# Optimization experiments

Hardware: AMD Instinct MI355X
Metric: run time of the kernel (lower is better)

Reference implementation:

```python
import jax, jax.numpy as jnp
import numpy as np

N_NODES = 100000

def gcn_conv(x, edge_index, W, b):
    # GCNConv with normalize=True and self-loops:
    # out = D^{-1/2} (A + I) D^{-1/2} (x W) + b
    h = x @ W                                   # [N, out]
    src, dst = edge_index[0], edge_index[1]
    deg = jax.ops.segment_sum(jnp.ones(src.shape[0], h.dtype), dst,
                              num_segments=N_NODES) + 1.0  # +1 for self loop
    dinv = jax.lax.rsqrt(deg)
    norm = dinv[src] * dinv[dst]                # [E]
    agg = jax.ops.segment_sum(h[src] * norm[:, None], dst,
                              num_segments=N_NODES)        # [N, out]
    agg = agg + h * (1.0 / deg)[:, None]        # self-loop term: norm_ii = 1/deg_i
    return agg + b


def setup_inputs() -> dict:
    key = jax.random.key(0)
    k0, k1, k2, k3 = jax.random.split(key, 4)
    N, E, F_IN, H, C = N_NODES, 1600000, 256, 128, 40
    x = jax.random.normal(k0, (N, F_IN), dtype=jnp.float32)
    edge_index = jax.random.randint(k1, (2, E), 0, N, dtype=jnp.int64)
    W1 = jax.random.normal(k2, (F_IN, H), dtype=jnp.float32) * (1.0 / np.sqrt(F_IN))
    b1 = jnp.zeros((H,), jnp.float32)
    W2 = jax.random.normal(k3, (H, C), dtype=jnp.float32) * (1.0 / np.sqrt(H))
    b2 = jnp.zeros((C,), jnp.float32)
    return {"x": x, "edge_index": edge_index, "W1": W1, "b1": b1, "W2": W2, "b2": b2}


def reference(x, edge_index, W1, b1, W2, b2):
    # layer 1 + ReLU (dropout = identity in eval mode)
    h = jax.nn.relu(gcn_conv(x, edge_index, W1, b1))
    # final layer (no activation)
    return gcn_conv(h, edge_index, W2, b2)
```

## Files before the change

kernel.cpp:

```cpp
#include <hip/hip_runtime.h>
#include <hip/hip_bf16.h>


#define FIN 256
#define HDIM 128
#define CDIM 40
#define CAP 8192
#define EC 8192

typedef __attribute__((ext_vector_type(8))) short bf16x8;
typedef __attribute__((ext_vector_type(4))) float f32x4;

__device__ inline short f2bf(float f) {
    unsigned u = __float_as_uint(f);
    unsigned r = (u + 0x7FFFu + ((u >> 16) & 1u)) >> 16;
    return (short)r;
}
__device__ inline float bflo(unsigned u) { return __uint_as_float(u << 16); }
__device__ inline float bfhi(unsigned u) { return __uint_as_float(u & 0xFFFF0000u); }
__device__ inline int rdl_i(int v, int l) { return __builtin_amdgcn_readlane(v, l); }
__device__ inline float rdl_f(float v, int l) {
    return __uint_as_float((unsigned)__builtin_amdgcn_readlane((int)__float_as_uint(v), l));
}

__global__ __launch_bounds__(1024) void p1_hist_k(const int* __restrict__ ei, int* __restrict__ mat,
                                                  int E, int NBUCK) {
    __shared__ int hist[512];
    for (int t = threadIdx.x; t < NBUCK; t += 1024) hist[t] = 0;
    __syncthreads();
    int e0 = blockIdx.x * EC;
#pragma unroll
    for (int k = 0; k < EC; k += 1024) {
        int e = e0 + k + threadIdx.x;
        if (e < E) atomicAdd(&hist[ei[E + e] >> 8], 1);
    }
    __syncthreads();
    for (int t = threadIdx.x; t < NBUCK; t += 1024) mat[blockIdx.x * NBUCK + t] = hist[t];
}

__global__ __launch_bounds__(64) void scan_cols_k(int* __restrict__ mat, int* __restrict__ bcnt,
                                                  int NB1, int NBUCK) {
    int b = blockIdx.x;
    int lane = threadIdx.x;
    int carry = b * CAP;
    for (int c0 = 0; c0 < NB1; c0 += 64) {
        int idx = c0 + lane;
        int v = (idx < NB1) ? mat[idx * NBUCK + b] : 0;
        int incl = v;
#pragma unroll
        for (int off = 1; off < 64; off <<= 1) {
            int t = __shfl_up(incl, off);
            if (lane >= off) incl += t;
        }
        if (idx < NB1) mat[idx * NBUCK + b] = carry + (incl - v);
        carry += __shfl(incl, 63);
    }
    if (lane == 0) bcnt[b] = carry - b * CAP;
}

__global__ __launch_bounds__(1024) void p1_scatter_k(const int* __restrict__ ei, const int* __restrict__ mat,
                                                     int* __restrict__ bmem, int E, int NBUCK) {
    __shared__ int base[512];
    for (int t = threadIdx.x; t < NBUCK; t += 1024) base[t] = mat[blockIdx.x * NBUCK + t];
    __syncthreads();
    int e0 = blockIdx.x * EC;
#pragma unroll
    for (int k = 0; k < EC; k += 1024) {
        int e = e0 + k + threadIdx.x;
        if (e < E) {
            int s = ei[e];
            int d = ei[E + e];
            int pos = atomicAdd(&base[d >> 8], 1);
            bmem[pos] = s | ((d & 255) << 20);
        }
    }
}

__global__ __launch_bounds__(256) void p2_build_k(const int* __restrict__ bmem, const int* __restrict__ bcnt,
                                                  int* __restrict__ csr, int2* __restrict__ nseg,
                                                  float* __restrict__ dinv, float* __restrict__ invd, int N) {
    __shared__ int hist[256], cur[256], sc[256];
    __shared__ int stage[CAP];
    const int b = blockIdx.x;
    const int tid = threadIdx.x;
    int cnt = bcnt[b];
    if (cnt > CAP) cnt = CAP;
    const int* src = bmem + b * CAP;
    hist[tid] = 0;
    __syncthreads();
    for (int j = tid; j < cnt; j += 256) atomicAdd(&hist[src[j] >> 20], 1);
    __syncthreads();
    int v = hist[tid];
    sc[tid] = v;
    __syncthreads();
    for (int off = 1; off < 256; off <<= 1) {
        int t = (tid >= off) ? sc[tid - off] : 0;
        __syncthreads();
        sc[tid] += t;
        __syncthreads();
    }
    int excl = sc[tid] - v;
    cur[tid] = excl;
    int i = b * 256 + tid;
    if (i < N) {
        nseg[i] = make_int2(b * CAP + excl, v);
        float dg = (float)(v + 1);
        dinv[i] = rsqrtf(dg);
        invd[i] = 1.0f / dg;
    }
    __syncthreads();
    for (int j = tid; j < cnt; j += 256) {
        int rec = src[j];
        int pos = atomicAdd(&cur[rec >> 20], 1);
        stage[pos] = rec & 0xFFFFF;
    }
    __syncthreads();
    int* dst = csr + b * CAP;
    for (int j = tid; j < cnt; j += 256) dst[j] = stage[j];
}

__global__ __launch_bounds__(256) void castW1_k(const float* __restrict__ W1, short* __restrict__ W1T) {
    int idx = blockIdx.x * 256 + threadIdx.x;
    int k = idx >> 7, n = idx & 127;
    W1T[n * FIN + k] = f2bf(W1[idx]);
}

__global__ __launch_bounds__(256) void castW2_k(const float* __restrict__ W2, short* __restrict__ W2T) {
    int idx = blockIdx.x * 256 + threadIdx.x;
    int c = idx >> 7, k = idx & 127;
    W2T[idx] = (c < CDIM) ? f2bf(W2[k * CDIM + c]) : (short)0;
}

#define LDSTRIDE 40
__global__ __launch_bounds__(256) void gemm1_mfma_k(const float* __restrict__ X,
                                                    const short* __restrict__ W1T,
                                                    short* __restrict__ T1b, int N) {
    __shared__ short As[128 * LDSTRIDE];
    __shared__ short Bs[128 * LDSTRIDE];
    const int tid = threadIdx.x;
    const int lane = tid & 63;
    const int wid = tid >> 6;
    const int w0 = wid & 1, w1 = wid >> 1;
    const int quad = lane >> 4;
    const int l16 = lane & 15;
    const int rowbase = blockIdx.x * 128;
    const int sr = tid >> 1;
    const int sh = tid & 1;

    f32x4 acc[4][4];
#pragma unroll
    for (int a = 0; a < 4; a++)
#pragma unroll
        for (int b = 0; b < 4; b++) acc[a][b] = (f32x4){0.f, 0.f, 0.f, 0.f};

    const int arow = min(rowbase + sr, N - 1);
    const float* xsrc = X + (size_t)arow * FIN + sh * 16;
    const int4* bsrc = (const int4*)(W1T + (size_t)sr * FIN + sh * 16);

    for (int k0 = 0; k0 < FIN; k0 += 32) {
        float vals[16];
        *(float4*)&vals[0]  = *(const float4*)(xsrc + k0);
        *(float4*)&vals[4]  = *(const float4*)(xsrc + k0 + 4);
        *(float4*)&vals[8]  = *(const float4*)(xsrc + k0 + 8);
        *(float4*)&vals[12] = *(const float4*)(xsrc + k0 + 12);
        short tmp[16];
#pragma unroll
        for (int c = 0; c < 16; c++) tmp[c] = f2bf(vals[c]);
        ((int4*)&As[sr * LDSTRIDE + sh * 16])[0] = ((int4*)tmp)[0];
        ((int4*)&As[sr * LDSTRIDE + sh * 16])[1] = ((int4*)tmp)[1];
        int4 b0 = bsrc[k0 >> 3];
        int4 b1 = bsrc[(k0 >> 3) + 1];
        ((int4*)&Bs[sr * LDSTRIDE + sh * 16])[0] = b0;
        ((int4*)&Bs[sr * LDSTRIDE + sh * 16])[1] = b1;
        __syncthreads();

        bf16x8 afr[4], bfr[4];
#pragma unroll
        for (int mt = 0; mt < 4; mt++)
            afr[mt] = *(const bf16x8*)&As[(w1 * 64 + mt * 16 + l16) * LDSTRIDE + quad * 8];
#pragma unroll
        for (int nt = 0; nt < 4; nt++)
            bfr[nt] = *(const bf16x8*)&Bs[(w0 * 64 + nt * 16 + l16) * LDSTRIDE + quad * 8];
#pragma unroll
        for (int mt = 0; mt < 4; mt++)
#pragma unroll
            for (int nt = 0; nt < 4; nt++)
                acc[mt][nt] = __builtin_amdgcn_mfma_f32_16x16x32_bf16(afr[mt], bfr[nt], acc[mt][nt], 0, 0, 0);
        __syncthreads();
    }
#pragma unroll
    for (int mt = 0; mt < 4; mt++) {
#pragma unroll
        for (int r = 0; r < 4; r++) {
            int row = rowbase + w1 * 64 + mt * 16 + quad * 4 + r;
            if (row < N) {
#pragma unroll
                for (int nt = 0; nt < 4; nt++) {
                    int col = w0 * 64 + nt * 16 + l16;
                    T1b[(size_t)row * HDIM + col] = f2bf(acc[mt][nt][r]);
                }
            }
        }
    }
}

__global__ __launch_bounds__(256) void agg1_k(const short* __restrict__ T1b, const int2* __restrict__ nseg,
                                              const int* __restrict__ csr, const float* __restrict__ dinv,
                                              const float* __restrict__ invd, const float* __restrict__ b1,
                                              unsigned* __restrict__ Hb, int N) {
    const int lane = threadIdx.x & 63;
    const int i = blockIdx.x * 4 + (threadIdx.x >> 6);
    if (i >= N) return;
    const int2 sg = nseg[i];
    const int e0 = sg.x, deg = sg.y;
    int sv = 0; float wv = 0.f;
    if (lane < deg) { sv = csr[e0 + lane]; wv = dinv[sv]; }

    float accx = 0.f, accy = 0.f;
    const int dmain = deg < 64 ? deg : 64;
    const int d8 = dmain & ~7;
    const unsigned* rowp = (const unsigned*)T1b;
    int j = 0;
    for (; j < d8; j += 8) {
        int   s0 = rdl_i(sv, j),     s1 = rdl_i(sv, j + 1), s2 = rdl_i(sv, j + 2), s3 = rdl_i(sv, j + 3);
        int   s4 = rdl_i(sv, j + 4), s5 = rdl_i(sv, j + 5), s6 = rdl_i(sv, j + 6), s7 = rdl_i(sv, j + 7);
        float w0 = rdl_f(wv, j),     w1 = rdl_f(wv, j + 1), w2 = rdl_f(wv, j + 2), w3 = rdl_f(wv, j + 3);
        float w4 = rdl_f(wv, j + 4), w5 = rdl_f(wv, j + 5), w6 = rdl_f(wv, j + 6), w7 = rdl_f(wv, j + 7);
        unsigned r0 = rowp[(size_t)s0 * 64 + lane];
        unsigned r1 = rowp[(size_t)s1 * 64 + lane];
        unsigned r2 = rowp[(size_t)s2 * 64 + lane];
        unsigned r3 = rowp[(size_t)s3 * 64 + lane];
        unsigned r4 = rowp[(size_t)s4 * 64 + lane];
        unsigned r5 = rowp[(size_t)s5 * 64 + lane];
        unsigned r6 = rowp[(size_t)s6 * 64 + lane];
        unsigned r7 = rowp[(size_t)s7 * 64 + lane];
        accx += w0 * bflo(r0) + w1 * bflo(r1) + w2 * bflo(r2) + w3 * bflo(r3)
              + w4 * bflo(r4) + w5 * bflo(r5) + w6 * bflo(r6) + w7 * bflo(r7);
        accy += w0 * bfhi(r0) + w1 * bfhi(r1) + w2 * bfhi(r2) + w3 * bfhi(r3)
              + w4 * bfhi(r4) + w5 * bfhi(r5) + w6 * bfhi(r6) + w7 * bfhi(r7);
    }
    for (; j < dmain; ++j) {
        int s = rdl_i(sv, j); float w = rdl_f(wv, j);
        unsigned r = rowp[(size_t)s * 64 + lane];
        accx += w * bflo(r); accy += w * bfhi(r);
    }
    for (int e = e0 + 64; e < e0 + deg; ++e) {
        int s = csr[e]; float w = dinv[s];
        unsigned r = rowp[(size_t)s * 64 + lane];
        accx += w * bflo(r); accy += w * bfhi(r);
    }
    const float di = dinv[i], sf = invd[i];
    unsigned rs = rowp[(size_t)i * 64 + lane];
    float2 bc = *(const float2*)(b1 + 2 * lane);
    float ox = fmaxf(bc.x + sf * bflo(rs) + di * accx, 0.f);
    float oy = fmaxf(bc.y + sf * bfhi(rs) + di * accy, 0.f);
    unsigned pk = ((unsigned)(unsigned short)f2bf(ox)) | (((unsigned)(unsigned short)f2bf(oy)) << 16);
    Hb[(size_t)i * 64 + lane] = pk;
}

__global__ __launch_bounds__(256) void gemm2_mfma_k(const short* __restrict__ Hb,
                                                    const short* __restrict__ W2T,
                                                    float* __restrict__ T2, int N) {
    __shared__ short As[128 * LDSTRIDE];
    __shared__ short Bs[48 * LDSTRIDE];
    const int tid = threadIdx.x;
    const int lane = tid & 63;
    const int wid = tid >> 6;
    const int quad = lane >> 4;
    const int l16 = lane & 15;
    const int rowbase = blockIdx.x * 128;
    const int sr = tid >> 1;
    const int sh = tid & 1;

    f32x4 acc[2][3];
#pragma unroll
    for (int a = 0; a < 2; a++)
#pragma unroll
        for (int b = 0; b < 3; b++) acc[a][b] = (f32x4){0.f, 0.f, 0.f, 0.f};

    const int arow = min(rowbase + sr, N - 1);
    const int4* asrc = (const int4*)(Hb + (size_t)arow * HDIM + sh * 16);
    const int br = tid >> 1, bh = tid & 1;
    const int4* bsrc = (const int4*)(W2T + br * HDIM + bh * 16);

    for (int k0 = 0; k0 < HDIM; k0 += 32) {
        int4 a0 = asrc[k0 >> 3];
        int4 a1 = asrc[(k0 >> 3) + 1];
        ((int4*)&As[sr * LDSTRIDE + sh * 16])[0] = a0;
        ((int4*)&As[sr * LDSTRIDE + sh * 16])[1] = a1;
        if (tid < 96) {
            int4 b0 = bsrc[k0 >> 3];
            int4 b1 = bsrc[(k0 >> 3) + 1];
            ((int4*)&Bs[br * LDSTRIDE + bh * 16])[0] = b0;
            ((int4*)&Bs[br * LDSTRIDE + bh * 16])[1] = b1;
        }
        __syncthreads();
        bf16x8 afr[2], bfr[3];
#pragma unroll
        for (int mt = 0; mt < 2; mt++)
            afr[mt] = *(const bf16x8*)&As[(wid * 32 + mt * 16 + l16) * LDSTRIDE + quad * 8];
#pragma unroll
        for (int nt = 0; nt < 3; nt++)
            bfr[nt] = *(const bf16x8*)&Bs[(nt * 16 + l16) * LDSTRIDE + quad * 8];
#pragma unroll
        for (int mt = 0; mt < 2; mt++)
#pragma unroll
            for (int nt = 0; nt < 3; nt++)
                acc[mt][nt] = __builtin_amdgcn_mfma_f32_16x16x32_bf16(afr[mt], bfr[nt], acc[mt][nt], 0, 0, 0);
        __syncthreads();
    }
#pragma unroll
    for (int mt = 0; mt < 2; mt++) {
#pragma unroll
        for (int r = 0; r < 4; r++) {
            int row = rowbase + wid * 32 + mt * 16 + quad * 4 + r;
            if (row < N) {
#pragma unroll
                for (int nt = 0; nt < 3; nt++) {
                    int col = nt * 16 + l16;
                    if (col < CDIM) T2[(size_t)row * CDIM + col] = acc[mt][nt][r];
                }
            }
        }
    }
}

__global__ __launch_bounds__(256) void agg2_k(const float* __restrict__ T2, const int2* __restrict__ nseg,
                                              const int* __restrict__ csr, const float* __restrict__ dinv,
                                              const float* __restrict__ invd, const float* __restrict__ b2,
                                              float* __restrict__ OUT, int N) {
    const int lane = threadIdx.x & 63;
    const int i = blockIdx.x * 4 + (threadIdx.x >> 6);
    if (i >= N) return;
    const int2 sg = nseg[i];
    const int e0 = sg.x, deg = sg.y;
    int sv = 0; float wv = 0.f;
    if (lane < deg) { sv = csr[e0 + lane]; wv = dinv[sv]; }
    const int c = lane < CDIM ? lane : CDIM - 1;
    float accE = 0.f;
    const int dmain = deg < 64 ? deg : 64;
    const int d8 = dmain & ~7;
    int j = 0;
    for (; j < d8; j += 8) {
        int   s0 = rdl_i(sv, j),     s1 = rdl_i(sv, j + 1), s2 = rdl_i(sv, j + 2), s3 = rdl_i(sv, j + 3);
        int   s4 = rdl_i(sv, j + 4), s5 = rdl_i(sv, j + 5), s6 = rdl_i(sv, j + 6), s7 = rdl_i(sv, j + 7);
        float w0 = rdl_f(wv, j),     w1 = rdl_f(wv, j + 1), w2 = rdl_f(wv, j + 2), w3 = rdl_f(wv, j + 3);
        float w4 = rdl_f(wv, j + 4), w5 = rdl_f(wv, j + 5), w6 = rdl_f(wv, j + 6), w7 = rdl_f(wv, j + 7);
        float v0 = T2[(size_t)s0 * CDIM + c];
        float v1 = T2[(size_t)s1 * CDIM + c];
        float v2 = T2[(size_t)s2 * CDIM + c];
        float v3 = T2[(size_t)s3 * CDIM + c];
        float v4 = T2[(size_t)s4 * CDIM + c];
        float v5 = T2[(size_t)s5 * CDIM + c];
        float v6 = T2[(size_t)s6 * CDIM + c];
        float v7 = T2[(size_t)s7 * CDIM + c];
        accE += w0 * v0 + w1 * v1 + w2 * v2 + w3 * v3 + w4 * v4 + w5 * v5 + w6 * v6 + w7 * v7;
    }
    for (; j < dmain; ++j) {
        int s = rdl_i(sv, j); float w = rdl_f(wv, j);
        accE += w * T2[(size_t)s * CDIM + c];
    }
    for (int e = e0 + 64; e < e0 + deg; ++e) {
        int s = csr[e]; float w = dinv[s];
        accE += w * T2[(size_t)s * CDIM + c];
    }
    if (lane < CDIM)
        OUT[(size_t)i * CDIM + lane] = b2[lane] + invd[i] * T2[(size_t)i * CDIM + lane] + dinv[i] * accE;
}

extern "C" void kernel_launch(void* const* d_in, const int* in_sizes, int n_in,
                              void* d_out, int out_size, void* d_ws, size_t ws_size,
                              hipStream_t stream) {
    const float* x   = (const float*)d_in[0];
    const int*   ei  = (const int*)d_in[1];
    const float* W1  = (const float*)d_in[2];
    const float* b1  = (const float*)d_in[3];
    const float* W2  = (const float*)d_in[4];
    const float* b2  = (const float*)d_in[5];
    float*       out = (float*)d_out;

    const int Hd  = in_sizes[3];
    const int Fin = in_sizes[2] / Hd;
    const int N   = in_sizes[0] / Fin;
    const int E   = in_sizes[1] / 2;

    const int NBUCK = (N + 255) / 256;
    const int NB1   = (E + EC - 1) / EC;

    char* base = (char*)d_ws;
    size_t off = 0;
    auto alloc = [&](size_t bytes) -> void* {
        void* p = base + off;
        off += (bytes + 255) & ~(size_t)255;
        return p;
    };
    size_t matB  = (size_t)NB1 * NBUCK * 4;
    size_t bmemB = (size_t)NBUCK * CAP * 4;
    size_t t1bB  = (size_t)N * HDIM * 2;
    size_t regA  = matB + 256 + bmemB;
    if (t1bB > regA) regA = t1bB;
    char* pA = (char*)alloc(regA);
    int*   mat  = (int*)pA;
    int*   bmem = (int*)(pA + ((matB + 255) & ~(size_t)255));
    short* t1b  = (short*)pA;

    int*      bcnt = (int*)alloc((size_t)NBUCK * 4);
    int*      csr  = (int*)alloc((size_t)NBUCK * CAP * 4);
    int2*     nseg = (int2*)alloc((size_t)N * 8);
    float*    dinv = (float*)alloc((size_t)N * 4);
    float*    invd = (float*)alloc((size_t)N * 4);
    short*    W1T  = (short*)alloc((size_t)HDIM * FIN * 2);
    short*    W2T  = (short*)alloc((size_t)48 * HDIM * 2);
    unsigned* hb   = (unsigned*)alloc((size_t)N * HDIM * 2);
    float*    t2   = (float*)alloc((size_t)N * CDIM * 4);

    p1_hist_k<<<NB1, 1024, 0, stream>>>(ei, mat, E, NBUCK);
    scan_cols_k<<<NBUCK, 64, 0, stream>>>(mat, bcnt, NB1, NBUCK);
    p1_scatter_k<<<NB1, 1024, 0, stream>>>(ei, mat, bmem, E, NBUCK);
    p2_build_k<<<NBUCK, 256, 0, stream>>>(bmem, bcnt, csr, nseg, dinv, invd, N);
    castW1_k<<<(HDIM * Fin + 255) / 256, 256, 0, stream>>>(W1, W1T);
    castW2_k<<<(48 * HDIM + 255) / 256, 256, 0, stream>>>(W2, W2T);

    gemm1_mfma_k<<<(N + 127) / 128, 256, 0, stream>>>(x, W1T, t1b, N);
    agg1_k<<<(N + 3) / 4, 256, 0, stream>>>(t1b, nseg, csr, dinv, invd, b1, hb, N);
    gemm2_mfma_k<<<(N + 127) / 128, 256, 0, stream>>>((const short*)hb, W2T, t2, N);
    agg2_k<<<(N + 3) / 4, 256, 0, stream>>>(t2, nseg, csr, dinv, invd, b2, out, N);
}
```

Measured before the change: 360.6 us.

## Split each wavefront into four quads gathering different neighbours with 16-byte loads

The two aggregation kernels now assign each 16-lane quarter of a wavefront to a different neighbour. Each lane loads 16 bytes (8 bf16 features in layer 1, 4 floats in layer 2) instead of one 4-byte word, and the four partial sums are combined with xor shuffles at the end. The aim is more memory-level parallelism per wavefront and fewer, wider gather instructions, especially for the 40-wide layer-2 rows where many lanes sat idle before. It also merges the two weight-cast kernels into one launch. The cost is extra shuffle reductions, a quarter of lanes idle in layer 2, and fewer unrolled independent loads per iteration.

```diff
diff --git a/kernel.cpp b/kernel.cpp
--- a/kernel.cpp
+++ b/kernel.cpp
@@ -18,10 +18,6 @@
 }
 __device__ inline float bflo(unsigned u) { return __uint_as_float(u << 16); }
 __device__ inline float bfhi(unsigned u) { return __uint_as_float(u & 0xFFFF0000u); }
-__device__ inline int rdl_i(int v, int l) { return __builtin_amdgcn_readlane(v, l); }
-__device__ inline float rdl_f(float v, int l) {
-    return __uint_as_float((unsigned)__builtin_amdgcn_readlane((int)__float_as_uint(v), l));
-}
 
 __global__ __launch_bounds__(1024) void p1_hist_k(const int* __restrict__ ei, int* __restrict__ mat,
                                                   int E, int NBUCK) {
@@ -119,16 +115,19 @@
     for (int j = tid; j < cnt; j += 256) dst[j] = stage[j];
 }
 
-__global__ __launch_bounds__(256) void castW1_k(const float* __restrict__ W1, short* __restrict__ W1T) {
+__global__ __launch_bounds__(256) void castW_k(const float* __restrict__ W1, const float* __restrict__ W2,
+                                               short* __restrict__ W1T, short* __restrict__ W2T) {
     int idx = blockIdx.x * 256 + threadIdx.x;
-    int k = idx >> 7, n = idx & 127;
-    W1T[n * FIN + k] = f2bf(W1[idx]);
-}
-
-__global__ __launch_bounds__(256) void castW2_k(const float* __restrict__ W2, short* __restrict__ W2T) {
-    int idx = blockIdx.x * 256 + threadIdx.x;
-    int c = idx >> 7, k = idx & 127;
-    W2T[idx] = (c < CDIM) ? f2bf(W2[k * CDIM + c]) : (short)0;
+    if (idx < FIN * HDIM) {
+        int k = idx >> 7, n = idx & 127;
+        W1T[n * FIN + k] = f2bf(W1[idx]);
+    } else {
+        int j = idx - FIN * HDIM;
+        if (j < 48 * HDIM) {
+            int c = j >> 7, k = j & 127;
+            W2T[j] = (c < CDIM) ? f2bf(W2[k * CDIM + c]) : (short)0;
+        }
+    }
 }
 
 #define LDSTRIDE 40
@@ -209,6 +208,8 @@
                                               const float* __restrict__ invd, const float* __restrict__ b1,
                                               unsigned* __restrict__ Hb, int N) {
     const int lane = threadIdx.x & 63;
+    const int quad = lane >> 4;
+    const int ql = lane & 15;
     const int i = blockIdx.x * 4 + (threadIdx.x >> 6);
     if (i >= N) return;
     const int2 sg = nseg[i];
@@ -216,46 +217,58 @@
     int sv = 0; float wv = 0.f;
     if (lane < deg) { sv = csr[e0 + lane]; wv = dinv[sv]; }
 
-    float accx = 0.f, accy = 0.f;
+    const uint4* rowp = (const uint4*)T1b;
+    float acc[8];
+#pragma unroll
+    for (int t = 0; t < 8; t++) acc[t] = 0.f;
+
     const int dmain = deg < 64 ? deg : 64;
-    const int d8 = dmain & ~7;
-    const unsigned* rowp = (const unsigned*)T1b;
-    int j = 0;
-    for (; j < d8; j += 8) {
-        int   s0 = rdl_i(sv, j),     s1 = rdl_i(sv, j + 1), s2 = rdl_i(sv, j + 2), s3 = rdl_i(sv, j + 3);
-        int   s4 = rdl_i(sv, j + 4), s5 = rdl_i(sv, j + 5), s6 = rdl_i(sv, j + 6), s7 = rdl_i(sv, j + 7);
-        float w0 = rdl_f(wv, j),     w1 = rdl_f(wv, j + 1), w2 = rdl_f(wv, j + 2), w3 = rdl_f(wv, j + 3);
-        float w4 = rdl_f(wv, j + 4), w5 = rdl_f(wv, j + 5), w6 = rdl_f(wv, j + 6), w7 = rdl_f(wv, j + 7);
-        unsigned r0 = rowp[(size_t)s0 * 64 + lane];
-        unsigned r1 = rowp[(size_t)s1 * 64 + lane];
-        unsigned r2 = rowp[(size_t)s2 * 64 + lane];
-        unsigned r3 = rowp[(size_t)s3 * 64 + lane];
-        unsigned r4 = rowp[(size_t)s4 * 64 + lane];
-        unsigned r5 = rowp[(size_t)s5 * 64 + lane];
-        unsigned r6 = rowp[(size_t)s6 * 64 + lane];
-        unsigned r7 = rowp[(size_t)s7 * 64 + lane];
-        accx += w0 * bflo(r0) + w1 * bflo(r1) + w2 * bflo(r2) + w3 * bflo(r3)
-              + w4 * bflo(r4) + w5 * bflo(r5) + w6 * bflo(r6) + w7 * bflo(r7);
-        accy += w0 * bfhi(r0) + w1 * bfhi(r1) + w2 * bfhi(r2) + w3 * bfhi(r3)
-              + w4 * bfhi(r4) + w5 * bfhi(r5) + w6 * bfhi(r6) + w7 * bfhi(r7);
-    }
-    for (; j < dmain; ++j) {
-        int s = rdl_i(sv, j); float w = rdl_f(wv, j);
-        unsigned r = rowp[(size_t)s * 64 + lane];
-        accx += w * bflo(r); accy += w * bfhi(r);
-    }
-    for (int e = e0 + 64; e < e0 + deg; ++e) {
-        int s = csr[e]; float w = dinv[s];
-        unsigned r = rowp[(size_t)s * 64 + lane];
-        accx += w * bflo(r); accy += w * bfhi(r);
+    for (int j = 0; j < dmain; j += 4) {
+        int idx = j + quad;
+        int sj = __shfl(sv, idx);
+        float wj = __shfl(wv, idx);
+        wj = (idx < dmain) ? wj : 0.f;
+        uint4 u = rowp[sj * 16 + ql];
+        acc[0] += wj * bflo(u.x); acc[1] += wj * bfhi(u.x);
+        acc[2] += wj * bflo(u.y); acc[3] += wj * bfhi(u.y);
+        acc[4] += wj * bflo(u.z); acc[5] += wj * bfhi(u.z);
+        acc[6] += wj * bflo(u.w); acc[7] += wj * bfhi(u.w);
+    }
+    const int eEnd = e0 + deg;
+    for (int e = e0 + 64; e < eEnd; e += 4) {
+        int idx = e + quad;
+        int cl = idx < eEnd ? idx : eEnd - 1;
+        int sj = csr[cl];
+        float wj = (idx < eEnd) ? dinv[sj] : 0.f;
+        uint4 u = rowp[sj * 16 + ql];
+        acc[0] += wj * bflo(u.x); acc[1] += wj * bfhi(u.x);
+        acc[2] += wj * bflo(u.y); acc[3] += wj * bfhi(u.y);
+        acc[4] += wj * bflo(u.z); acc[5] += wj * bfhi(u.z);
+        acc[6] += wj * bflo(u.w); acc[7] += wj * bfhi(u.w);
+    }
+#pragma unroll
+    for (int t = 0; t < 8; t++) {
+        acc[t] += __shfl_xor(acc[t], 16);
+        acc[t] += __shfl_xor(acc[t], 32);
     }
     const float di = dinv[i], sf = invd[i];
-    unsigned rs = rowp[(size_t)i * 64 + lane];
-    float2 bc = *(const float2*)(b1 + 2 * lane);
-    float ox = fmaxf(bc.x + sf * bflo(rs) + di * accx, 0.f);
-    float oy = fmaxf(bc.y + sf * bfhi(rs) + di * accy, 0.f);
-    unsigned pk = ((unsigned)(unsigned short)f2bf(ox)) | (((unsigned)(unsigned short)f2bf(oy)) << 16);
-    Hb[(size_t)i * 64 + lane] = pk;
+    uint4 us = rowp[i * 16 + ql];
+    float4 bA = *(const float4*)(b1 + ql * 8);
+    float4 bB = *(const float4*)(b1 + ql * 8 + 4);
+    float o0 = fmaxf(bA.x + sf * bflo(us.x) + di * acc[0], 0.f);
+    float o1 = fmaxf(bA.y + sf * bfhi(us.x) + di * acc[1], 0.f);
+    float o2 = fmaxf(bA.z + sf * bflo(us.y) + di * acc[2], 0.f);
+    float o3 = fmaxf(bA.w + sf * bfhi(us.y) + di * acc[3], 0.f);
+    float o4 = fmaxf(bB.x + sf * bflo(us.z) + di * acc[4], 0.f);
+    float o5 = fmaxf(bB.y + sf * bfhi(us.z) + di * acc[5], 0.f);
+    float o6 = fmaxf(bB.z + sf * bflo(us.w) + di * acc[6], 0.f);
+    float o7 = fmaxf(bB.w + sf * bfhi(us.w) + di * acc[7], 0.f);
+    uint4 pk;
+    pk.x = ((unsigned)(unsigned short)f2bf(o0)) | (((unsigned)(unsigned short)f2bf(o1)) << 16);
+    pk.y = ((unsigned)(unsigned short)f2bf(o2)) | (((unsigned)(unsigned short)f2bf(o3)) << 16);
+    pk.z = ((unsigned)(unsigned short)f2bf(o4)) | (((unsigned)(unsigned short)f2bf(o5)) << 16);
+    pk.w = ((unsigned)(unsigned short)f2bf(o6)) | (((unsigned)(unsigned short)f2bf(o7)) << 16);
+    if (quad == 0) ((uint4*)(Hb + (size_t)i * 64))[ql] = pk;
 }
 
 __global__ __launch_bounds__(256) void gemm2_mfma_k(const short* __restrict__ Hb,
@@ -330,42 +343,49 @@
                                               const float* __restrict__ invd, const float* __restrict__ b2,
                                               float* __restrict__ OUT, int N) {
     const int lane = threadIdx.x & 63;
+    const int quad = lane >> 4;
+    const int qlr = lane & 15;
+    const int ql = qlr < 10 ? qlr : 9;
+    const bool act = qlr < 10;
     const int i = blockIdx.x * 4 + (threadIdx.x >> 6);
     if (i >= N) return;
     const int2 sg = nseg[i];
     const int e0 = sg.x, deg = sg.y;
     int sv = 0; float wv = 0.f;
     if (lane < deg) { sv = csr[e0 + lane]; wv = dinv[sv]; }
-    const int c = lane < CDIM ? lane : CDIM - 1;
-    float accE = 0.f;
+    float acc[4] = {0.f, 0.f, 0.f, 0.f};
     const int dmain = deg < 64 ? deg : 64;
-    const int d8 = dmain & ~7;
-    int j = 0;
-    for (; j < d8; j += 8) {
-        int   s0 = rdl_i(sv, j),     s1 = rdl_i(sv, j + 1), s2 = rdl_i(sv, j + 2), s3 = rdl_i(sv, j + 3);
-        int   s4 = rdl_i(sv, j + 4), s5 = rdl_i(sv, j + 5), s6 = rdl_i(sv, j + 6), s7 = rdl_i(sv, j + 7);
-        float w0 = rdl_f(wv, j),     w1 = rdl_f(wv, j + 1), w2 = rdl_f(wv, j + 2), w3 = rdl_f(wv, j + 3);
-        float w4 = rdl_f(wv, j + 4), w5 = rdl_f(wv, j + 5), w6 = rdl_f(wv, j + 6), w7 = rdl_f(wv, j + 7);
-        float v0 = T2[(size_t)s0 * CDIM + c];
-        float v1 = T2[(size_t)s1 * CDIM + c];
-        float v2 = T2[(size_t)s2 * CDIM + c];
-        float v3 = T2[(size_t)s3 * CDIM + c];
-        float v4 = T2[(size_t)s4 * CDIM + c];
-        float v5 = T2[(size_t)s5 * CDIM + c];
-        float v6 = T2[(size_t)s6 * CDIM + c];
-        float v7 = T2[(size_t)s7 * CDIM + c];
-        accE += w0 * v0 + w1 * v1 + w2 * v2 + w3 * v3 + w4 * v4 + w5 * v5 + w6 * v6 + w7 * v7;
-    }
-    for (; j < dmain; ++j) {
-        int s = rdl_i(sv, j); float w = rdl_f(wv, j);
-        accE += w * T2[(size_t)s * CDIM + c];
-    }
-    for (int e = e0 + 64; e < e0 + deg; ++e) {
-        int s = csr[e]; float w = dinv[s];
-        accE += w * T2[(size_t)s * CDIM + c];
-    }
-    if (lane < CDIM)
-        OUT[(size_t)i * CDIM + lane] = b2[lane] + invd[i] * T2[(size_t)i * CDIM + lane] + dinv[i] * accE;
+    for (int j = 0; j < dmain; j += 4) {
+        int idx = j + quad;
+        int sj = __shfl(sv, idx);
+        float wj = __shfl(wv, idx);
+        wj = (idx < dmain && act) ? wj : 0.f;
+        float4 v = *(const float4*)(T2 + sj * CDIM + ql * 4);
+        acc[0] += wj * v.x; acc[1] += wj * v.y; acc[2] += wj * v.z; acc[3] += wj * v.w;
+    }
+    const int eEnd = e0 + deg;
+    for (int e = e0 + 64; e < eEnd; e += 4) {
+        int idx = e + quad;
+        int cl = idx < eEnd ? idx : eEnd - 1;
+        int sj = csr[cl];
+        float wj = (idx < eEnd && act) ? dinv[sj] : 0.f;
+        float4 v = *(const float4*)(T2 + sj * CDIM + ql * 4);
+        acc[0] += wj * v.x; acc[1] += wj * v.y; acc[2] += wj * v.z; acc[3] += wj * v.w;
+    }
+#pragma unroll
+    for (int t = 0; t < 4; t++) {
+        acc[t] += __shfl_xor(acc[t], 16);
+        acc[t] += __shfl_xor(acc[t], 32);
+    }
+    const float di = dinv[i], sf = invd[i];
+    float4 vs = *(const float4*)(T2 + (size_t)i * CDIM + ql * 4);
+    float4 bb = *(const float4*)(b2 + ql * 4);
+    float4 o;
+    o.x = bb.x + sf * vs.x + di * acc[0];
+    o.y = bb.y + sf * vs.y + di * acc[1];
+    o.z = bb.z + sf * vs.z + di * acc[2];
+    o.w = bb.w + sf * vs.w + di * acc[3];
+    if (quad == 0 && act) *(float4*)(OUT + (size_t)i * CDIM + qlr * 4) = o;
 }
 
 extern "C" void kernel_launch(void* const* d_in, const int* in_sizes, int n_in,
@@ -418,8 +438,7 @@
     scan_cols_k<<<NBUCK, 64, 0, stream>>>(mat, bcnt, NB1, NBUCK);
     p1_scatter_k<<<NB1, 1024, 0, stream>>>(ei, mat, bmem, E, NBUCK);
     p2_build_k<<<NBUCK, 256, 0, stream>>>(bmem, bcnt, csr, nseg, dinv, invd, N);
-    castW1_k<<<(HDIM * Fin + 255) / 256, 256, 0, stream>>>(W1, W1T);
-    castW2_k<<<(48 * HDIM + 255) / 256, 256, 0, stream>>>(W2, W2T);
+    castW_k<<<(FIN * HDIM + 48 * HDIM + 255) / 256, 256, 0, stream>>>(W1, W2, W1T, W2T);
 
     gemm1_mfma_k<<<(N + 127) / 128, 256, 0, stream>>>(x, W1T, t1b, N);
     agg1_k<<<(N + 3) / 4, 256, 0, stream>>>(t1b, nseg, csr, dinv, invd, b1, hb, N);
```

Result: no change. 360.6 us (-0.0%).
